# Kernel optimization log

Measured on AMD Instinct MI355X. Metric: run time of the kernel, lower is better.

The kernel has to match this reference:

```python
import jax, jax.numpy as jnp
import numpy as np

B, S, IN, H, T, OUT = 128, 336, 64, 1024, 96, 1


def _lstm_step(h, c, x, W_ih, W_hh, b_ih, b_hh):
    # PyTorch LSTM cell: gates in (i, f, g, o) order
    g = x @ W_ih.T + b_ih + h @ W_hh.T + b_hh  # [B, 4H]
    i, f, gg, o = jnp.split(g, 4, axis=-1)
    c_new = jax.nn.sigmoid(f) * c + jax.nn.sigmoid(i) * jnp.tanh(gg)
    h_new = jax.nn.sigmoid(o) * jnp.tanh(c_new)
    return h_new, c_new


def setup_inputs() -> dict:
    key = jax.random.key(0)
    ks = jax.random.split(key, 12)
    s = 0.05
    return {
        "src": jax.random.normal(ks[0], (B, S, IN), jnp.float32),
        "enc_W_ih": jax.random.normal(ks[1], (4 * H, IN), jnp.float32) * s,
        "enc_W_hh": jax.random.normal(ks[2], (4 * H, H), jnp.float32) * s,
        "enc_b_ih": jax.random.normal(ks[3], (4 * H,), jnp.float32) * s,
        "enc_b_hh": jax.random.normal(ks[4], (4 * H,), jnp.float32) * s,
        "dec_W_ih": jax.random.normal(ks[5], (4 * H, OUT + H), jnp.float32) * s,
        "dec_W_hh": jax.random.normal(ks[6], (4 * H, H), jnp.float32) * s,
        "dec_b_ih": jax.random.normal(ks[7], (4 * H,), jnp.float32) * s,
        "dec_b_hh": jax.random.normal(ks[8], (4 * H,), jnp.float32) * s,
        "attn_W": jax.random.normal(ks[9], (H, H), jnp.float32) * s,
        "fc_W": jax.random.normal(ks[10], (OUT, H), jnp.float32) * s,
        "fc_b": jax.random.normal(ks[11], (OUT,), jnp.float32) * s,
        "target_len": T,
    }


def reference(src, enc_W_ih, enc_W_hh, enc_b_ih, enc_b_hh,
              dec_W_ih, dec_W_hh, dec_b_ih, dec_b_hh,
              attn_W, fc_W, fc_b, target_len):
    batch = src.shape[0]
    hdim = enc_W_hh.shape[1]

    # ---- Encoder: single-layer LSTM over src, batch_first ----
    def enc_step(carry, x_t):
        h, c = carry
        h, c = _lstm_step(h, c, x_t, enc_W_ih, enc_W_hh, enc_b_ih, enc_b_hh)
        return (h, c), h

    h0 = jnp.zeros((batch, hdim), src.dtype)
    c0 = jnp.zeros((batch, hdim), src.dtype)
    (h_enc, c_enc), enc_hs = jax.lax.scan(enc_step, (h0, c0),
                                          jnp.swapaxes(src, 0, 1))
    encoder_outputs = jnp.swapaxes(enc_hs, 0, 1)  # [B, S, H]

    def dec_step(carry, _):
        h, c, prev_y = carry
        q = h @ attn_W.T                                      # [B, H]
        energy = jnp.einsum('bh,bsh->bs', q, encoder_outputs)  # [B, S]
        w = jax.nn.softmax(energy, axis=-1)
        ctx = jnp.einsum('bs,bsh->bh', w, encoder_outputs)     # [B, H]
        x = jnp.concatenate([prev_y, ctx], axis=-1)            # [B, OUT+H]
        h, c = _lstm_step(h, c, x, dec_W_ih, dec_W_hh, dec_b_ih, dec_b_hh)
        pred = h @ fc_W.T + fc_b                               # [B, OUT]
        prev_y = jax.lax.stop_gradient(pred)                   # pred.detach()
        return (h, c, prev_y), pred

    prev_y0 = jnp.zeros((batch, fc_W.shape[0]), src.dtype)
    _, preds = jax.lax.scan(dec_step, (h_enc, c_enc, prev_y0), None,
                            length=target_len)
    return jnp.swapaxes(preds, 0, 1)  # [B, target_len, OUT]
```

## Files before the change

kernel.cpp:

```cpp
#include <hip/hip_runtime.h>
#include <math.h>

#define Bn   128
#define Sn   336
#define INd  64
#define Hn   1024
#define Tn   96
#define G4   4096
#define KCE  34
#define KCD  65
#define KCQ  32
#define NBLK 256
#define SHALF 168

typedef __attribute__((ext_vector_type(8))) short short8;
typedef __attribute__((ext_vector_type(4))) float floatx4;
typedef __attribute__((ext_vector_type(4))) unsigned int uintx4;
typedef unsigned long long u64t;

__device__ __forceinline__ float sigmoidf_(float x){ return 1.0f/(1.0f+expf(-x)); }

__device__ __forceinline__ unsigned short f2bf(float f){
    union { float f; unsigned u; } v; v.f = f;
    unsigned r = v.u + 0x7fffu + ((v.u >> 16) & 1u);
    return (unsigned short)(r >> 16);
}
__device__ __forceinline__ float bflo(unsigned u){ union{unsigned u; float f;} v; v.u = u << 16;        return v.f; }
__device__ __forceinline__ float bfhi(unsigned u){ union{unsigned u; float f;} v; v.u = u & 0xffff0000u; return v.f; }
__device__ __forceinline__ void unpack8v(uintx4 v, float* f){
    f[0]=bflo(v.x); f[1]=bfhi(v.x); f[2]=bflo(v.y); f[3]=bfhi(v.y);
    f[4]=bflo(v.z); f[5]=bfhi(v.z); f[6]=bflo(v.w); f[7]=bfhi(v.w);
}

union Frag16 { u64t q[2]; short8 s8; uintx4 u4; };
union F2 { u64t q; float f[2]; };

__device__ __forceinline__ short8 ld_cg_s8(const unsigned short* p){
    Frag16 r;
    r.q[0] = __hip_atomic_load((const u64t*)p,     __ATOMIC_RELAXED, __HIP_MEMORY_SCOPE_AGENT);
    r.q[1] = __hip_atomic_load((const u64t*)p + 1, __ATOMIC_RELAXED, __HIP_MEMORY_SCOPE_AGENT);
    return r.s8;
}
__device__ __forceinline__ uintx4 ld_cg_u4(const unsigned short* p){
    Frag16 r;
    r.q[0] = __hip_atomic_load((const u64t*)p,     __ATOMIC_RELAXED, __HIP_MEMORY_SCOPE_AGENT);
    r.q[1] = __hip_atomic_load((const u64t*)p + 1, __ATOMIC_RELAXED, __HIP_MEMORY_SCOPE_AGENT);
    return r.u4;
}
__device__ __forceinline__ void st_cg16(unsigned short* p, unsigned short v){
    asm volatile("global_store_short %0, %1, off sc0 sc1" :: "v"(p), "v"((unsigned)v) : "memory");
}
__device__ __forceinline__ void st_cg32(unsigned short* p, unsigned v){
    asm volatile("global_store_dword %0, %1, off sc0 sc1" :: "v"(p), "v"(v) : "memory");
}
__device__ __forceinline__ void st_cg64(float* p, float a, float b){
    F2 v; v.f[0] = a; v.f[1] = b;
    __hip_atomic_store((u64t*)p, v.q, __ATOMIC_RELAXED, __HIP_MEMORY_SCOPE_AGENT);
}
__device__ __forceinline__ F2 ld_cg64(const float* p){
    F2 v; v.q = __hip_atomic_load((const u64t*)p, __ATOMIC_RELAXED, __HIP_MEMORY_SCOPE_AGENT);
    return v;
}

__device__ __forceinline__ void gbar2(unsigned* bb, int g, bool rep, unsigned step){
    asm volatile("s_waitcnt vmcnt(0)" ::: "memory");
    __syncthreads();
    if (threadIdx.x == 0){
        __hip_atomic_fetch_add(bb + g*32, 1u, __ATOMIC_RELAXED, __HIP_MEMORY_SCOPE_AGENT);
        if (rep){
            while (__hip_atomic_load(bb + g*32, __ATOMIC_RELAXED, __HIP_MEMORY_SCOPE_AGENT) < step*32u)
                __builtin_amdgcn_s_sleep(1);
            __hip_atomic_fetch_add(bb + 256, 1u, __ATOMIC_RELAXED, __HIP_MEMORY_SCOPE_AGENT);
            while (__hip_atomic_load(bb + 256, __ATOMIC_RELAXED, __HIP_MEMORY_SCOPE_AGENT) < step*8u)
                __builtin_amdgcn_s_sleep(1);
            __hip_atomic_store(bb + 512 + g*32, step, __ATOMIC_RELAXED, __HIP_MEMORY_SCOPE_AGENT);
        } else {
            while (__hip_atomic_load(bb + 512 + g*32, __ATOMIC_RELAXED, __HIP_MEMORY_SCOPE_AGENT) < step)
                __builtin_amdgcn_s_sleep(1);
        }
    }
    __syncthreads();
}

__global__ void pack_encf(const float* __restrict__ Wih, const float* __restrict__ Whh,
                          const float* __restrict__ bih, const float* __restrict__ bhh,
                          unsigned short* __restrict__ Wp, float* __restrict__ bc){
    long n = (long)256*KCE*512;
    for (long idx = (long)blockIdx.x*256 + threadIdx.x; idx < n; idx += (long)gridDim.x*256){
        int j = (int)(idx & 7), l = (int)((idx >> 3) & 63);
        int kc = (int)((idx >> 9) % KCE);
        int s  = (int)(idx / (KCE*512));
        int c = l & 15, kg = l >> 4;
        int k = kc*32 + kg*8 + j;
        int gate = s & 3, unit = (s >> 2)*16 + c;
        int orig = gate*Hn + unit;
        float v = (k < INd) ? Wih[orig*INd + k] : Whh[(size_t)orig*Hn + (k - INd)];
        Wp[idx] = f2bf(v);
    }
    int tid = blockIdx.x*256 + threadIdx.x;
    if (tid < G4){
        int g = (tid >> 4) & 3, u = (tid >> 6)*16 + (tid & 15);
        int orig = g*Hn + u;
        bc[tid] = bih[orig] + bhh[orig];
    }
}

__global__ void pack_decf(const float* __restrict__ Wih, const float* __restrict__ Whh,
                          const float* __restrict__ bih, const float* __restrict__ bhh,
                          unsigned short* __restrict__ Wp, float* __restrict__ bc){
    long n = (long)256*KCD*512;
    for (long idx = (long)blockIdx.x*256 + threadIdx.x; idx < n; idx += (long)gridDim.x*256){
        int j = (int)(idx & 7), l = (int)((idx >> 3) & 63);
        int kc = (int)((idx >> 9) % KCD);
        int s  = (int)(idx / (KCD*512));
        int c = l & 15, kg = l >> 4;
        int k = kc*32 + kg*8 + j;
        int gate = s & 3, unit = (s >> 2)*16 + c;
        int orig = gate*Hn + unit;
        float v;
        if (k < Hn)          v = Wih[(size_t)orig*(Hn+1) + 1 + k];
        else if (k < 2*Hn)   v = Whh[(size_t)orig*Hn + (k - Hn)];
        else if (k == 2*Hn)  v = Wih[(size_t)orig*(Hn+1)];
        else                 v = 0.0f;
        Wp[idx] = f2bf(v);
    }
    int tid = blockIdx.x*256 + threadIdx.x;
    if (tid < G4){
        int g = (tid >> 4) & 3, u = (tid >> 6)*16 + (tid & 15);
        int orig = g*Hn + u;
        bc[tid] = bih[orig] + bhh[orig];
    }
}

__global__ void pack_attnf(const float* __restrict__ w, unsigned short* __restrict__ Wp){
    int n = 64*KCQ*512;
    for (int idx = blockIdx.x*256 + threadIdx.x; idx < n; idx += gridDim.x*256){
        int j = idx & 7, l = (idx >> 3) & 63;
        int kc = (idx >> 9) & 31;
        int s  = idx >> 14;
        int nn = s*16 + (l & 15);
        int k = kc*32 + (l >> 4)*8 + j;
        Wp[idx] = f2bf(w[(size_t)nn*Hn + k]);
    }
}

__global__ void conv_srcf(const float* __restrict__ s, unsigned short* __restrict__ d){
    int n = Sn*8*2*512;
    for (int idx = blockIdx.x*256 + threadIdx.x; idx < n; idx += gridDim.x*256){
        int j = idx & 7, l = (idx >> 3) & 63;
        int kc = (idx >> 9) & 1, rg = (idx >> 10) & 7, t = idx >> 13;
        int b = rg*16 + (l & 15);
        int k = kc*32 + (l >> 4)*8 + j;
        d[idx] = f2bf(s[((size_t)b*Sn + t)*INd + k]);
    }
}

__global__ void init_ws(unsigned short* __restrict__ hf0, float* __restrict__ cbuf,
                        unsigned short* __restrict__ A0, unsigned short* __restrict__ A1,
                        unsigned* __restrict__ bars){
    int t0 = blockIdx.x*256 + threadIdx.x;
    if (t0 < 2048) bars[t0] = 0;
    for (int i = t0; i < 8*KCD*512; i += gridDim.x*256){
        A0[i] = 0; A1[i] = 0;
        if (i < 8*32*512) hf0[i] = 0;
        if (i < Bn*Hn) cbuf[i] = 0.0f;
    }
}

__device__ __forceinline__ void swz(int b, int& x, int& y){
    int xcd = b & 7, li = b >> 3;
    y = xcd*8 + (li & 7);
    x = li >> 3;
}

__device__ __forceinline__ float fcdot(const unsigned short* __restrict__ hplain,
                                       const float* __restrict__ fcW, int b, int l){
    const unsigned short* hp = hplain + (size_t)b*Hn + l*16;
    uintx4 h0 = ld_cg_u4(hp), h1 = ld_cg_u4(hp + 8);
    float hf[16]; unpack8v(h0, hf); unpack8v(h1, hf + 8);
    float p = 0.0f;
    #pragma unroll
    for (int i = 0; i < 16; i++) p = fmaf(hf[i], fcW[l*16 + i], p);
    #pragma unroll
    for (int off = 32; off; off >>= 1) p += __shfl_down(p, off);
    return p;
}

__global__ __launch_bounds__(256, 1)
void enc_loop(const unsigned short* __restrict__ srcfrag,
              const unsigned short* __restrict__ Wf,
              const float* __restrict__ bc, float* __restrict__ cbuf,
              unsigned short* __restrict__ hf0,
              unsigned short* __restrict__ hf1,
              unsigned short* __restrict__ enco,
              unsigned short* __restrict__ adec0,
              unsigned* __restrict__ bar)
{
    __shared__ float red[2][16][65];
    const int tid = threadIdx.x, l = tid & 63, w = tid >> 6;
    const int rgw = w & 1, kh = w >> 1;
    int x, y; swz(blockIdx.x, x, y);
    const int g = blockIdx.x & 7;
    const bool rep = (blockIdx.x >> 3) == 0;
    const int rg = x*2 + rgw;
    const int m0 = rg*16;
    const unsigned short* Bf = Wf + (size_t)(4*y)*KCE*512 + l*8;

    const int col = l & 15, q = l >> 4;
    const int u = y*16 + col;
    const float bi  = bc[y*64 + col];
    const float bf_ = bc[y*64 + 16 + col];
    const float bg  = bc[y*64 + 32 + col];
    const float bo  = bc[y*64 + 48 + col];
    const int lsh = ((u >> 3) & 3) * 16;

    unsigned bstep = 0;
    for (int t = 0; t < Sn; t++){
        const unsigned short* hin = (t & 1) ? hf1 : hf0;
        unsigned short* hout      = (t & 1) ? hf0 : hf1;
        const unsigned short* Ah = hin + (size_t)rg*32*512 + l*8;
        floatx4 acc0={0,0,0,0}, acc1={0,0,0,0}, acc2={0,0,0,0}, acc3={0,0,0,0};

        if (kh == 0){
            short8 ah[15];
            #pragma unroll
            for (int hc = 0; hc < 15; hc++) ah[hc] = ld_cg_s8(Ah + hc*512);
            const unsigned short* Ax = srcfrag + ((size_t)t*8 + rg)*2*512 + l*8;
            #pragma unroll
            for (int kc = 0; kc < 2; kc++){
                short8 a  = *(const short8*)(Ax + kc*512);
                short8 b0 = *(const short8*)(Bf + (0*KCE + kc)*512);
                short8 b1 = *(const short8*)(Bf + (1*KCE + kc)*512);
                short8 b2 = *(const short8*)(Bf + (2*KCE + kc)*512);
                short8 b3 = *(const short8*)(Bf + (3*KCE + kc)*512);
                acc0 = __builtin_amdgcn_mfma_f32_16x16x32_bf16(a, b0, acc0, 0, 0, 0);
                acc1 = __builtin_amdgcn_mfma_f32_16x16x32_bf16(a, b1, acc1, 0, 0, 0);
                acc2 = __builtin_amdgcn_mfma_f32_16x16x32_bf16(a, b2, acc2, 0, 0, 0);
                acc3 = __builtin_amdgcn_mfma_f32_16x16x32_bf16(a, b3, acc3, 0, 0, 0);
            }
            #pragma unroll
            for (int hc = 0; hc < 15; hc++){
                short8 b0 = *(const short8*)(Bf + (0*KCE + hc + 2)*512);
                short8 b1 = *(const short8*)(Bf + (1*KCE + hc + 2)*512);
                short8 b2 = *(const short8*)(Bf + (2*KCE + hc + 2)*512);
                short8 b3 = *(const short8*)(Bf + (3*KCE + hc + 2)*512);
                acc0 = __builtin_amdgcn_mfma_f32_16x16x32_bf16(ah[hc], b0, acc0, 0, 0, 0);
                acc1 = __builtin_amdgcn_mfma_f32_16x16x32_bf16(ah[hc], b1, acc1, 0, 0, 0);
                acc2 = __builtin_amdgcn_mfma_f32_16x16x32_bf16(ah[hc], b2, acc2, 0, 0, 0);
                acc3 = __builtin_amdgcn_mfma_f32_16x16x32_bf16(ah[hc], b3, acc3, 0, 0, 0);
            }
        } else {
            short8 ah[17];
            #pragma unroll
            for (int i = 0; i < 17; i++) ah[i] = ld_cg_s8(Ah + (15 + i)*512);
            #pragma unroll
            for (int i = 0; i < 17; i++){
                short8 b0 = *(const short8*)(Bf + (0*KCE + i + 17)*512);
                short8 b1 = *(const short8*)(Bf + (1*KCE + i + 17)*512);
                short8 b2 = *(const short8*)(Bf + (2*KCE + i + 17)*512);
                short8 b3 = *(const short8*)(Bf + (3*KCE + i + 17)*512);
                acc0 = __builtin_amdgcn_mfma_f32_16x16x32_bf16(ah[i], b0, acc0, 0, 0, 0);
                acc1 = __builtin_amdgcn_mfma_f32_16x16x32_bf16(ah[i], b1, acc1, 0, 0, 0);
                acc2 = __builtin_amdgcn_mfma_f32_16x16x32_bf16(ah[i], b2, acc2, 0, 0, 0);
                acc3 = __builtin_amdgcn_mfma_f32_16x16x32_bf16(ah[i], b3, acc3, 0, 0, 0);
            }
            #pragma unroll
            for (int r = 0; r < 4; r++){
                red[rgw][ 0 + r][l] = acc0[r];
                red[rgw][ 4 + r][l] = acc1[r];
                red[rgw][ 8 + r][l] = acc2[r];
                red[rgw][12 + r][l] = acc3[r];
            }
        }
        __syncthreads();
        if (kh == 0){
            #pragma unroll
            for (int r = 0; r < 4; r++){
                acc0[r] += red[rgw][ 0 + r][l];
                acc1[r] += red[rgw][ 4 + r][l];
                acc2[r] += red[rgw][ 8 + r][l];
                acc3[r] += red[rgw][12 + r][l];
            }
            #pragma unroll
            for (int r = 0; r < 4; r++){
                const int m = m0 + q*4 + r;
                float gi = acc0[r] + bi;
                float gf = acc1[r] + bf_;
                float gg = acc2[r] + bg;
                float go = acc3[r] + bo;
                float co = cbuf[(size_t)m*Hn + u];
                float cn = sigmoidf_(gf)*co + sigmoidf_(gi)*tanhf(gg);
                float hv = sigmoidf_(go)*tanhf(cn);
                cbuf[(size_t)m*Hn + u] = cn;
                unsigned short hb = f2bf(hv);
                const int lanep = (q*4 + r) + lsh;
                st_cg16(hout + (((size_t)rg*32 + (u >> 5))*64 + lanep)*8 + (u & 7), hb);
                enco[((size_t)m*Sn + t)*Hn + u] = hb;
                if (t == Sn-1) adec0[(((size_t)rg*KCD + 32 + (u >> 5))*64 + lanep)*8 + (u & 7)] = hb;
            }
        }
        bstep++; gbar2(bar, g, rep, bstep);
    }
}

__global__ __launch_bounds__(512, 1)
void dec_loop(unsigned short* __restrict__ A0, unsigned short* __restrict__ A1,
              const unsigned short* __restrict__ Wdec,
              const float* __restrict__ bdec, float* __restrict__ cbuf,
              const unsigned short* __restrict__ Watt,
              unsigned short* __restrict__ qbf,
              const unsigned short* __restrict__ enco,
              unsigned short* __restrict__ hplain,
              float* __restrict__ pctx,
              float* __restrict__ pml,
              const float* __restrict__ fcW, const float* __restrict__ fcb,
              float* __restrict__ out, unsigned* __restrict__ bar)
{
    __shared__ float smem[8224];
    const int tid = threadIdx.x, l = tid & 63, w = tid >> 6;
    const int rgw = w & 1, ks = w >> 1;
    int x, y; swz(blockIdx.x, x, y);
    const int g = blockIdx.x & 7;
    const bool rep = (blockIdx.x >> 3) == 0;
    const int rg = x*2 + rgw, m0 = rg*16;
    const unsigned short* Bf = Wdec + (size_t)(4*y)*KCD*512 + l*8;
    const unsigned short* Bq = Watt + (size_t)y*KCQ*512 + l*8;

    const int col = l & 15, q4 = l >> 4;
    const int u = y*16 + col;
    const float bi  = bdec[y*64 + col];
    const float bf_ = bdec[y*64 + 16 + col];
    const float bg  = bdec[y*64 + 32 + col];
    const float bo  = bdec[y*64 + 48 + col];
    const int lsh = ((u >> 3) & 3) * 16;
    const int ab   = blockIdx.x & 127;
    const int part = blockIdx.x >> 7;

    unsigned bstep = 0;
    for (int d = 0; d < Tn; d++){
        unsigned short* Ac = (d & 1) ? A1 : A0;
        unsigned short* An = (d & 1) ? A0 : A1;
        const unsigned short* Af = Ac + (size_t)rg*KCD*512 + l*8;

        floatx4 acc0={0,0,0,0}, acc1={0,0,0,0}, acc2={0,0,0,0}, acc3={0,0,0,0};
        {
            short8 aA[8];
            #pragma unroll
            for (int kk = 0; kk < 8; kk++)
                aA[kk] = ld_cg_s8(Af + (32 + ks*8 + kk)*512);
            floatx4 qa = {0,0,0,0};
            #pragma unroll
            for (int kk = 0; kk < 8; kk++){
                const int kc = 32 + ks*8 + kk;
                short8 b0 = *(const short8*)(Bf + (0*KCD + kc)*512);
                short8 b1 = *(const short8*)(Bf + (1*KCD + kc)*512);
                short8 b2 = *(const short8*)(Bf + (2*KCD + kc)*512);
                short8 b3 = *(const short8*)(Bf + (3*KCD + kc)*512);
                short8 bq = *(const short8*)(Bq + (ks*8 + kk)*512);
                acc0 = __builtin_amdgcn_mfma_f32_16x16x32_bf16(aA[kk], b0, acc0, 0, 0, 0);
                acc1 = __builtin_amdgcn_mfma_f32_16x16x32_bf16(aA[kk], b1, acc1, 0, 0, 0);
                acc2 = __builtin_amdgcn_mfma_f32_16x16x32_bf16(aA[kk], b2, acc2, 0, 0, 0);
                acc3 = __builtin_amdgcn_mfma_f32_16x16x32_bf16(aA[kk], b3, acc3, 0, 0, 0);
                qa   = __builtin_amdgcn_mfma_f32_16x16x32_bf16(aA[kk], bq, qa, 0, 0, 0);
            }
            #pragma unroll
            for (int r = 0; r < 4; r++) smem[(w*4 + r)*64 + l] = qa[r];
        }
        __syncthreads();
        if (ks == 0){
            #pragma unroll
            for (int r = 0; r < 4; r++){
                float s = smem[((0*2+rgw)*4 + r)*64 + l] + smem[((1*2+rgw)*4 + r)*64 + l]
                        + smem[((2*2+rgw)*4 + r)*64 + l] + smem[((3*2+rgw)*4 + r)*64 + l];
                st_cg16(qbf + (size_t)(m0 + q4*4 + r)*Hn + y*16 + col, f2bf(s));
            }
        }
        if (d > 0 && x == 0 && w >= 6){
            const int b = y*2 + (w & 1);
            float p = fcdot(hplain, fcW, b, l);
            if (l == 0){
                float pv = p + fcb[0];
                out[b*Tn + (d-1)] = pv;
                st_cg16(Ac + (((size_t)(b >> 4))*KCD + 64)*512 + (b & 15)*8, f2bf(pv));
            }
        }
        bstep++; gbar2(bar, g, rep, bstep);

        {
            float* ctxl = smem;
            float* mred = smem + 8192;
            float* lred = smem + 8200;
            float qv[16];
            {
                const unsigned short* qp = qbf + (size_t)ab*Hn + l*16;
                uintx4 q0 = ld_cg_u4(qp), q1 = ld_cg_u4(qp + 8);
                unpack8v(q0, qv); unpack8v(q1, qv + 8);
            }
            float mx = -1e30f, lsum = 0.0f;
            float cacc[16];
            #pragma unroll
            for (int i = 0; i < 16; i++) cacc[i] = 0.0f;

            const uintx4* ebase = (const uintx4*)(enco + (size_t)ab*Sn*Hn) + l*2;
            const int s0i = part*SHALF;
            for (int s = s0i + w; s < s0i + SHALF; s += 8){
                uintx4 e0 = ebase[(size_t)s*128];
                uintx4 e1 = ebase[(size_t)s*128 + 1];
                float ev[16];
                unpack8v(e0, ev); unpack8v(e1, ev + 8);
                float pt = 0.0f;
                #pragma unroll
                for (int i = 0; i < 16; i++) pt = fmaf(qv[i], ev[i], pt);
                #pragma unroll
                for (int off = 32; off; off >>= 1) pt += __shfl_down(pt, off);
                float e = __shfl(pt, 0);
                float mn = fmaxf(mx, e);
                float corr = expf(mx - mn);
                float p = expf(e - mn);
                lsum = lsum*corr + p;
                if (corr != 1.0f){
                    #pragma unroll
                    for (int i = 0; i < 16; i++) cacc[i] *= corr;
                }
                #pragma unroll
                for (int i = 0; i < 16; i++) cacc[i] = fmaf(p, ev[i], cacc[i]);
                mx = mn;
            }
            if (l == 0){ mred[w] = mx; lred[w] = lsum; }
            __syncthreads();
            float M = mred[0];
            #pragma unroll
            for (int k = 1; k < 8; k++) M = fmaxf(M, mred[k]);
            float corr2 = expf(mx - M);
            #pragma unroll
            for (int j = 0; j < 16; j++) ctxl[w*1024 + j*64 + l] = cacc[j]*corr2;
            __syncthreads();
            float L = 0.0f;
            #pragma unroll
            for (int k = 0; k < 8; k++) L += lred[k]*expf(mred[k] - M);

            const int u0 = 2*tid;
            float s0 = 0.0f, s1 = 0.0f;
            #pragma unroll
            for (int k = 0; k < 8; k++){
                s0 += ctxl[k*1024 + (u0 & 15)*64 + (u0 >> 4)];
                s1 += ctxl[k*1024 + ((u0+1) & 15)*64 + ((u0+1) >> 4)];
            }
            st_cg64(pctx + ((size_t)part*128 + ab)*1024 + u0, s0, s1);
            if (tid == 0) st_cg64(pml + ((size_t)part*128 + ab)*2, M, L);
        }
        bstep++; gbar2(bar, g, rep, bstep);

        if (blockIdx.x < Bn){
            const int b = blockIdx.x;
            F2 ml0 = ld_cg64(pml + (size_t)b*2);
            F2 ml1 = ld_cg64(pml + (size_t)(128 + b)*2);
            float M = fmaxf(ml0.f[0], ml1.f[0]);
            float w0 = expf(ml0.f[0] - M), w1 = expf(ml1.f[0] - M);
            float invL = 1.0f / (ml0.f[1]*w0 + ml1.f[1]*w1);
            const int u0 = 2*tid;
            F2 c0 = ld_cg64(pctx + (size_t)b*1024 + u0);
            F2 c1 = ld_cg64(pctx + ((size_t)128 + b)*1024 + u0);
            float v0 = (c0.f[0]*w0 + c1.f[0]*w1)*invL;
            float v1 = (c0.f[1]*w0 + c1.f[1]*w1)*invL;
            unsigned cvu = (unsigned)f2bf(v0) | ((unsigned)f2bf(v1) << 16);
            const int kcw = u0 >> 5;
            const int lanep2 = (b & 15) + ((u0 >> 3) & 3)*16;
            st_cg32(Ac + ((((size_t)(b >> 4))*KCD + kcw)*64 + lanep2)*8 + (u0 & 7), cvu);
        }
        bstep++; gbar2(bar, g, rep, bstep);

        {
            short8 aC[8];
            #pragma unroll
            for (int kk = 0; kk < 8; kk++)
                aC[kk] = ld_cg_s8(Af + (ks*8 + kk)*512);
            #pragma unroll
            for (int kk = 0; kk < 8; kk++){
                const int kc = ks*8 + kk;
                short8 b0 = *(const short8*)(Bf + (0*KCD + kc)*512);
                short8 b1 = *(const short8*)(Bf + (1*KCD + kc)*512);
                short8 b2 = *(const short8*)(Bf + (2*KCD + kc)*512);
                short8 b3 = *(const short8*)(Bf + (3*KCD + kc)*512);
                acc0 = __builtin_amdgcn_mfma_f32_16x16x32_bf16(aC[kk], b0, acc0, 0, 0, 0);
                acc1 = __builtin_amdgcn_mfma_f32_16x16x32_bf16(aC[kk], b1, acc1, 0, 0, 0);
                acc2 = __builtin_amdgcn_mfma_f32_16x16x32_bf16(aC[kk], b2, acc2, 0, 0, 0);
                acc3 = __builtin_amdgcn_mfma_f32_16x16x32_bf16(aC[kk], b3, acc3, 0, 0, 0);
            }
            if (ks == 3){
                short8 a  = ld_cg_s8(Af + 64*512);
                short8 b0 = *(const short8*)(Bf + (0*KCD + 64)*512);
                short8 b1 = *(const short8*)(Bf + (1*KCD + 64)*512);
                short8 b2 = *(const short8*)(Bf + (2*KCD + 64)*512);
                short8 b3 = *(const short8*)(Bf + (3*KCD + 64)*512);
                acc0 = __builtin_amdgcn_mfma_f32_16x16x32_bf16(a, b0, acc0, 0, 0, 0);
                acc1 = __builtin_amdgcn_mfma_f32_16x16x32_bf16(a, b1, acc1, 0, 0, 0);
                acc2 = __builtin_amdgcn_mfma_f32_16x16x32_bf16(a, b2, acc2, 0, 0, 0);
                acc3 = __builtin_amdgcn_mfma_f32_16x16x32_bf16(a, b3, acc3, 0, 0, 0);
            }
        }
        if (ks != 0){
            float* rp = smem + ((ks-1)*2 + rgw)*1024;
            #pragma unroll
            for (int r = 0; r < 4; r++){
                rp[( 0 + r)*64 + l] = acc0[r];
                rp[( 4 + r)*64 + l] = acc1[r];
                rp[( 8 + r)*64 + l] = acc2[r];
                rp[(12 + r)*64 + l] = acc3[r];
            }
        }
        __syncthreads();
        if (ks == 0){
            const float* r0 = smem + rgw*1024;
            const float* r1 = smem + (2 + rgw)*1024;
            const float* r2 = smem + (4 + rgw)*1024;
            #pragma unroll
            for (int r = 0; r < 4; r++){
                acc0[r] += r0[( 0+r)*64 + l] + r1[( 0+r)*64 + l] + r2[( 0+r)*64 + l];
                acc1[r] += r0[( 4+r)*64 + l] + r1[( 4+r)*64 + l] + r2[( 4+r)*64 + l];
                acc2[r] += r0[( 8+r)*64 + l] + r1[( 8+r)*64 + l] + r2[( 8+r)*64 + l];
                acc3[r] += r0[(12+r)*64 + l] + r1[(12+r)*64 + l] + r2[(12+r)*64 + l];
            }
            #pragma unroll
            for (int r = 0; r < 4; r++){
                const int m = m0 + q4*4 + r;
                float gi = acc0[r] + bi;
                float gf = acc1[r] + bf_;
                float gg = acc2[r] + bg;
                float go = acc3[r] + bo;
                float co = cbuf[(size_t)m*Hn + u];
                float cn = sigmoidf_(gf)*co + sigmoidf_(gi)*tanhf(gg);
                float hv = sigmoidf_(go)*tanhf(cn);
                cbuf[(size_t)m*Hn + u] = cn;
                unsigned short hb = f2bf(hv);
                const int lanep = (q4*4 + r) + lsh;
                st_cg16(An + (((size_t)rg*KCD + 32 + (u >> 5))*64 + lanep)*8 + (u & 7), hb);
                st_cg16(hplain + (size_t)m*Hn + u, hb);
            }
        }
        bstep++; gbar2(bar, g, rep, bstep);
    }

    if (x == 0 && w >= 6){
        const int b = y*2 + (w & 1);
        float p = fcdot(hplain, fcW, b, l);
        if (l == 0) out[b*Tn + (Tn - 1)] = p + fcb[0];
    }
}

extern "C" void kernel_launch(void* const* d_in, const int* in_sizes, int n_in,
                              void* d_out, int out_size, void* d_ws, size_t ws_size,
                              hipStream_t stream){
    const float* src  = (const float*)d_in[0];
    const float* eWih = (const float*)d_in[1];
    const float* eWhh = (const float*)d_in[2];
    const float* ebih = (const float*)d_in[3];
    const float* ebhh = (const float*)d_in[4];
    const float* dWih = (const float*)d_in[5];
    const float* dWhh = (const float*)d_in[6];
    const float* dbih = (const float*)d_in[7];
    const float* dbhh = (const float*)d_in[8];
    const float* attnW= (const float*)d_in[9];
    const float* fcW  = (const float*)d_in[10];
    const float* fcb  = (const float*)d_in[11];
    float* out = (float*)d_out;

    char* base = (char*)d_ws;
    auto alloc = [&](size_t bytes){ void* p = base; base += (bytes + 255) & ~255ull; return p; };
    unsigned short* Wencf = (unsigned short*)alloc((size_t)256*KCE*512*2);
    float*          benc  = (float*)alloc(G4*4);
    unsigned short* Wdecf = (unsigned short*)alloc((size_t)256*KCD*512*2);
    float*          bdec  = (float*)alloc(G4*4);
    unsigned short* Wattf = (unsigned short*)alloc((size_t)64*KCQ*512*2);
    unsigned short* srcf  = (unsigned short*)alloc((size_t)Sn*8*2*512*2);
    unsigned short* enco  = (unsigned short*)alloc((size_t)Bn*Sn*Hn*2);
    unsigned short* hf0   = (unsigned short*)alloc((size_t)8*32*512*2);
    unsigned short* hf1   = (unsigned short*)alloc((size_t)8*32*512*2);
    float*          cbuf  = (float*)alloc((size_t)Bn*Hn*4);
    unsigned short* A0f   = (unsigned short*)alloc((size_t)8*KCD*512*2);
    unsigned short* A1f   = (unsigned short*)alloc((size_t)8*KCD*512*2);
    unsigned short* qbf   = (unsigned short*)alloc((size_t)Bn*Hn*2);
    unsigned short* hplain= (unsigned short*)alloc((size_t)Bn*Hn*2);
    float*          pctx  = (float*)alloc((size_t)2*128*1024*4);
    float*          pml   = (float*)alloc((size_t)2*128*2*4);
    unsigned*       bars  = (unsigned*)alloc(2048*4);

    conv_srcf<<<2048, 256, 0, stream>>>(src, srcf);
    pack_encf<<<4096, 256, 0, stream>>>(eWih, eWhh, ebih, ebhh, Wencf, benc);
    pack_decf<<<8192, 256, 0, stream>>>(dWih, dWhh, dbih, dbhh, Wdecf, bdec);
    pack_attnf<<<1024, 256, 0, stream>>>(attnW, Wattf);
    init_ws<<<1040, 256, 0, stream>>>(hf0, cbuf, A0f, A1f, bars);

    enc_loop<<<NBLK, 256, 0, stream>>>(srcf, Wencf, benc, cbuf, hf0, hf1,
                                       enco, A0f, bars + 0);
    dec_loop<<<NBLK, 512, 0, stream>>>(A0f, A1f, Wdecf, bdec, cbuf, Wattf,
                                       qbf, enco, hplain, pctx, pml,
                                       fcW, fcb, out, bars + 1024);
}
```

Baseline: 9.691 ms.

## Replace hierarchical grid barrier, fuse ctx merge via last-arriver counter, unroll attention loads

Replaces the two-level counter-based grid barrier with a flag-per-block barrier where one wavefront of block 0 polls all 256 flags and publishes a release word. The separate context-merge phase and its grid barrier are removed: the last of the two partial blocks for each batch row, found with an atomic counter, merges the partial softmax results directly. The attention scan over encoder outputs is manually unrolled with four-deep register double buffering to overlap global loads with compute. This removes one grid-wide sync per decoder step and shortens barrier latency, but adds extra atomic traffic and a single-block polling bottleneck.

```diff
diff --git a/kernel.cpp b/kernel.cpp
--- a/kernel.cpp
+++ b/kernel.cpp
@@ -62,20 +62,29 @@
     return v;
 }
 
-__device__ __forceinline__ void gbar2(unsigned* bb, int g, bool rep, unsigned step){
+__device__ __forceinline__ void gbar3(unsigned* bb, unsigned step){
     asm volatile("s_waitcnt vmcnt(0)" ::: "memory");
     __syncthreads();
-    if (threadIdx.x == 0){
-        __hip_atomic_fetch_add(bb + g*32, 1u, __ATOMIC_RELAXED, __HIP_MEMORY_SCOPE_AGENT);
-        if (rep){
-            while (__hip_atomic_load(bb + g*32, __ATOMIC_RELAXED, __HIP_MEMORY_SCOPE_AGENT) < step*32u)
+    if (threadIdx.x == 0)
+        __hip_atomic_store(bb + blockIdx.x*32, step, __ATOMIC_RELAXED, __HIP_MEMORY_SCOPE_AGENT);
+    if (blockIdx.x == 0){
+        if (threadIdx.x < 64){
+            const int l = threadIdx.x;
+            for (;;){
+                unsigned a0 = __hip_atomic_load(bb + (l      )*32, __ATOMIC_RELAXED, __HIP_MEMORY_SCOPE_AGENT);
+                unsigned a1 = __hip_atomic_load(bb + (l +  64)*32, __ATOMIC_RELAXED, __HIP_MEMORY_SCOPE_AGENT);
+                unsigned a2 = __hip_atomic_load(bb + (l + 128)*32, __ATOMIC_RELAXED, __HIP_MEMORY_SCOPE_AGENT);
+                unsigned a3 = __hip_atomic_load(bb + (l + 192)*32, __ATOMIC_RELAXED, __HIP_MEMORY_SCOPE_AGENT);
+                int ok = (a0 >= step) && (a1 >= step) && (a2 >= step) && (a3 >= step);
+                if (__all(ok)) break;
                 __builtin_amdgcn_s_sleep(1);
-            __hip_atomic_fetch_add(bb + 256, 1u, __ATOMIC_RELAXED, __HIP_MEMORY_SCOPE_AGENT);
-            while (__hip_atomic_load(bb + 256, __ATOMIC_RELAXED, __HIP_MEMORY_SCOPE_AGENT) < step*8u)
-                __builtin_amdgcn_s_sleep(1);
-            __hip_atomic_store(bb + 512 + g*32, step, __ATOMIC_RELAXED, __HIP_MEMORY_SCOPE_AGENT);
-        } else {
-            while (__hip_atomic_load(bb + 512 + g*32, __ATOMIC_RELAXED, __HIP_MEMORY_SCOPE_AGENT) < step)
+            }
+            if (l == 0)
+                __hip_atomic_store(bb + 8192, step, __ATOMIC_RELAXED, __HIP_MEMORY_SCOPE_AGENT);
+        }
+    } else {
+        if (threadIdx.x == 0){
+            while (__hip_atomic_load(bb + 8192, __ATOMIC_RELAXED, __HIP_MEMORY_SCOPE_AGENT) < step)
                 __builtin_amdgcn_s_sleep(1);
         }
     }
@@ -157,13 +166,14 @@
 
 __global__ void init_ws(unsigned short* __restrict__ hf0, float* __restrict__ cbuf,
                         unsigned short* __restrict__ A0, unsigned short* __restrict__ A1,
-                        unsigned* __restrict__ bars){
+                        unsigned* __restrict__ bars, unsigned* __restrict__ pcnt){
     int t0 = blockIdx.x*256 + threadIdx.x;
-    if (t0 < 2048) bars[t0] = 0;
     for (int i = t0; i < 8*KCD*512; i += gridDim.x*256){
         A0[i] = 0; A1[i] = 0;
         if (i < 8*32*512) hf0[i] = 0;
         if (i < Bn*Hn) cbuf[i] = 0.0f;
+        if (i < 32768) bars[i] = 0;
+        if (i < 4096)  pcnt[i] = 0;
     }
 }
 
@@ -200,8 +210,6 @@
     const int tid = threadIdx.x, l = tid & 63, w = tid >> 6;
     const int rgw = w & 1, kh = w >> 1;
     int x, y; swz(blockIdx.x, x, y);
-    const int g = blockIdx.x & 7;
-    const bool rep = (blockIdx.x >> 3) == 0;
     const int rg = x*2 + rgw;
     const int m0 = rg*16;
     const unsigned short* Bf = Wf + (size_t)(4*y)*KCE*512 + l*8;
@@ -299,9 +307,25 @@
                 if (t == Sn-1) adec0[(((size_t)rg*KCD + 32 + (u >> 5))*64 + lanep)*8 + (u & 7)] = hb;
             }
         }
-        bstep++; gbar2(bar, g, rep, bstep);
-    }
-}
+        bstep++; gbar3(bar, bstep);
+    }
+}
+
+#define BLOAD(P, I) { const size_t s_ = (size_t)(sb + 8*(I)); \
+    buf_a##P = ebase[s_*128]; buf_b##P = ebase[s_*128 + 1]; }
+#define BPROC(P) { \
+    float ev[16]; unpack8v(buf_a##P, ev); unpack8v(buf_b##P, ev + 8); \
+    float pt = 0.0f; \
+    _Pragma("unroll") for (int i_ = 0; i_ < 16; i_++) pt = fmaf(qv[i_], ev[i_], pt); \
+    _Pragma("unroll") for (int o_ = 32; o_; o_ >>= 1) pt += __shfl_down(pt, o_); \
+    float e_ = __shfl(pt, 0); \
+    float mn_ = fmaxf(mx, e_); \
+    float corr_ = expf(mx - mn_); \
+    float p_ = expf(e_ - mn_); \
+    lsum = lsum*corr_ + p_; \
+    if (corr_ != 1.0f){ _Pragma("unroll") for (int i_ = 0; i_ < 16; i_++) cacc[i_] *= corr_; } \
+    _Pragma("unroll") for (int i_ = 0; i_ < 16; i_++) cacc[i_] = fmaf(p_, ev[i_], cacc[i_]); \
+    mx = mn_; }
 
 __global__ __launch_bounds__(512, 1)
 void dec_loop(unsigned short* __restrict__ A0, unsigned short* __restrict__ A1,
@@ -313,15 +337,15 @@
               unsigned short* __restrict__ hplain,
               float* __restrict__ pctx,
               float* __restrict__ pml,
+              unsigned* __restrict__ pcnt,
               const float* __restrict__ fcW, const float* __restrict__ fcb,
               float* __restrict__ out, unsigned* __restrict__ bar)
 {
     __shared__ float smem[8224];
+    __shared__ unsigned cflag_s;
     const int tid = threadIdx.x, l = tid & 63, w = tid >> 6;
     const int rgw = w & 1, ks = w >> 1;
     int x, y; swz(blockIdx.x, x, y);
-    const int g = blockIdx.x & 7;
-    const bool rep = (blockIdx.x >> 3) == 0;
     const int rg = x*2 + rgw, m0 = rg*16;
     const unsigned short* Bf = Wdec + (size_t)(4*y)*KCD*512 + l*8;
     const unsigned short* Bq = Watt + (size_t)y*KCQ*512 + l*8;
@@ -384,7 +408,7 @@
                 st_cg16(Ac + (((size_t)(b >> 4))*KCD + 64)*512 + (b & 15)*8, f2bf(pv));
             }
         }
-        bstep++; gbar2(bar, g, rep, bstep);
+        bstep++; gbar3(bar, bstep);
 
         {
             float* ctxl = smem;
@@ -402,30 +426,16 @@
             for (int i = 0; i < 16; i++) cacc[i] = 0.0f;
 
             const uintx4* ebase = (const uintx4*)(enco + (size_t)ab*Sn*Hn) + l*2;
-            const int s0i = part*SHALF;
-            for (int s = s0i + w; s < s0i + SHALF; s += 8){
-                uintx4 e0 = ebase[(size_t)s*128];
-                uintx4 e1 = ebase[(size_t)s*128 + 1];
-                float ev[16];
-                unpack8v(e0, ev); unpack8v(e1, ev + 8);
-                float pt = 0.0f;
-                #pragma unroll
-                for (int i = 0; i < 16; i++) pt = fmaf(qv[i], ev[i], pt);
-                #pragma unroll
-                for (int off = 32; off; off >>= 1) pt += __shfl_down(pt, off);
-                float e = __shfl(pt, 0);
-                float mn = fmaxf(mx, e);
-                float corr = expf(mx - mn);
-                float p = expf(e - mn);
-                lsum = lsum*corr + p;
-                if (corr != 1.0f){
-                    #pragma unroll
-                    for (int i = 0; i < 16; i++) cacc[i] *= corr;
-                }
-                #pragma unroll
-                for (int i = 0; i < 16; i++) cacc[i] = fmaf(p, ev[i], cacc[i]);
-                mx = mn;
-            }
+            const int sb = part*SHALF + w;
+            uintx4 buf_a0, buf_b0, buf_a1, buf_b1, buf_a2, buf_b2, buf_a3, buf_b3;
+            BLOAD(0,0)  BLOAD(1,1)  BLOAD(2,2)  BLOAD(3,3)
+            BPROC(0) BLOAD(0,4)  BPROC(1) BLOAD(1,5)  BPROC(2) BLOAD(2,6)  BPROC(3) BLOAD(3,7)
+            BPROC(0) BLOAD(0,8)  BPROC(1) BLOAD(1,9)  BPROC(2) BLOAD(2,10) BPROC(3) BLOAD(3,11)
+            BPROC(0) BLOAD(0,12) BPROC(1) BLOAD(1,13) BPROC(2) BLOAD(2,14) BPROC(3) BLOAD(3,15)
+            BPROC(0) BLOAD(0,16) BPROC(1) BLOAD(1,17) BPROC(2) BLOAD(2,18) BPROC(3) BLOAD(3,19)
+            BPROC(0) BLOAD(0,20) BPROC(1) BPROC(2) BPROC(3)
+            BPROC(0)
+
             if (l == 0){ mred[w] = mx; lred[w] = lsum; }
             __syncthreads();
             float M = mred[0];
@@ -447,28 +457,33 @@
                 s1 += ctxl[k*1024 + ((u0+1) & 15)*64 + ((u0+1) >> 4)];
             }
             st_cg64(pctx + ((size_t)part*128 + ab)*1024 + u0, s0, s1);
-            if (tid == 0) st_cg64(pml + ((size_t)part*128 + ab)*2, M, L);
-        }
-        bstep++; gbar2(bar, g, rep, bstep);
-
-        if (blockIdx.x < Bn){
-            const int b = blockIdx.x;
-            F2 ml0 = ld_cg64(pml + (size_t)b*2);
-            F2 ml1 = ld_cg64(pml + (size_t)(128 + b)*2);
-            float M = fmaxf(ml0.f[0], ml1.f[0]);
-            float w0 = expf(ml0.f[0] - M), w1 = expf(ml1.f[0] - M);
-            float invL = 1.0f / (ml0.f[1]*w0 + ml1.f[1]*w1);
-            const int u0 = 2*tid;
-            F2 c0 = ld_cg64(pctx + (size_t)b*1024 + u0);
-            F2 c1 = ld_cg64(pctx + ((size_t)128 + b)*1024 + u0);
-            float v0 = (c0.f[0]*w0 + c1.f[0]*w1)*invL;
-            float v1 = (c0.f[1]*w0 + c1.f[1]*w1)*invL;
-            unsigned cvu = (unsigned)f2bf(v0) | ((unsigned)f2bf(v1) << 16);
-            const int kcw = u0 >> 5;
-            const int lanep2 = (b & 15) + ((u0 >> 3) & 3)*16;
-            st_cg32(Ac + ((((size_t)(b >> 4))*KCD + kcw)*64 + lanep2)*8 + (u0 & 7), cvu);
-        }
-        bstep++; gbar2(bar, g, rep, bstep);
+            if (tid == 0) st_cg64(pml + ((size_t)part*128 + ab)*2, M, lsum*0.0f + L);
+
+            asm volatile("s_waitcnt vmcnt(0)" ::: "memory");
+            __syncthreads();
+            if (tid == 0){
+                unsigned old = __hip_atomic_fetch_add(pcnt + ab*32, 1u,
+                                  __ATOMIC_RELAXED, __HIP_MEMORY_SCOPE_AGENT);
+                cflag_s = (old == 2u*(unsigned)d + 1u);
+            }
+            __syncthreads();
+            if (cflag_s){
+                F2 ml0 = ld_cg64(pml + (size_t)ab*2);
+                F2 ml1 = ld_cg64(pml + (size_t)(128 + ab)*2);
+                float Mg = fmaxf(ml0.f[0], ml1.f[0]);
+                float w0 = expf(ml0.f[0] - Mg), w1 = expf(ml1.f[0] - Mg);
+                float invL = 1.0f / (ml0.f[1]*w0 + ml1.f[1]*w1);
+                F2 c0 = ld_cg64(pctx + (size_t)ab*1024 + u0);
+                F2 c1 = ld_cg64(pctx + ((size_t)128 + ab)*1024 + u0);
+                float v0 = (c0.f[0]*w0 + c1.f[0]*w1)*invL;
+                float v1 = (c0.f[1]*w0 + c1.f[1]*w1)*invL;
+                unsigned cvu = (unsigned)f2bf(v0) | ((unsigned)f2bf(v1) << 16);
+                const int kcw = u0 >> 5;
+                const int lanep2 = (ab & 15) + ((u0 >> 3) & 3)*16;
+                st_cg32(Ac + ((((size_t)(ab >> 4))*KCD + kcw)*64 + lanep2)*8 + (u0 & 7), cvu);
+            }
+        }
+        bstep++; gbar3(bar, bstep);
 
         {
             short8 aC[8];
@@ -538,7 +553,7 @@
                 st_cg16(hplain + (size_t)m*Hn + u, hb);
             }
         }
-        bstep++; gbar2(bar, g, rep, bstep);
+        bstep++; gbar3(bar, bstep);
     }
 
     if (x == 0 && w >= 6){
@@ -583,17 +598,18 @@
     unsigned short* hplain= (unsigned short*)alloc((size_t)Bn*Hn*2);
     float*          pctx  = (float*)alloc((size_t)2*128*1024*4);
     float*          pml   = (float*)alloc((size_t)2*128*2*4);
-    unsigned*       bars  = (unsigned*)alloc(2048*4);
+    unsigned*       bars  = (unsigned*)alloc((size_t)32768*4);
+    unsigned*       pcnt  = (unsigned*)alloc((size_t)4096*4);
 
     conv_srcf<<<2048, 256, 0, stream>>>(src, srcf);
     pack_encf<<<4096, 256, 0, stream>>>(eWih, eWhh, ebih, ebhh, Wencf, benc);
     pack_decf<<<8192, 256, 0, stream>>>(dWih, dWhh, dbih, dbhh, Wdecf, bdec);
     pack_attnf<<<1024, 256, 0, stream>>>(attnW, Wattf);
-    init_ws<<<1040, 256, 0, stream>>>(hf0, cbuf, A0f, A1f, bars);
+    init_ws<<<1040, 256, 0, stream>>>(hf0, cbuf, A0f, A1f, bars, pcnt);
 
     enc_loop<<<NBLK, 256, 0, stream>>>(srcf, Wencf, benc, cbuf, hf0, hf1,
-                                       enco, A0f, bars + 0);
+                                       enco, A0f, bars);
     dec_loop<<<NBLK, 512, 0, stream>>>(A0f, A1f, Wdecf, bdec, cbuf, Wattf,
-                                       qbf, enco, hplain, pctx, pml,
-                                       fcW, fcb, out, bars + 1024);
-}
+                                       qbf, enco, hplain, pctx, pml, pcnt,
+                                       fcW, fcb, out, bars + 16384);
+}
```

Result: slower. 10.87 ms (+12.2%).
